# Optimization experiments

Hardware: AMD Instinct MI355X
Metric: run time of the kernel (lower is better)

Reference implementation:

```python
import jax, jax.numpy as jnp
import numpy as np

N, E, DIM = 50000, 1600000, 64
EPS = 1e-5


def setup_inputs() -> dict:
    key = jax.random.key(0)
    ks = jax.random.split(key, 12)
    s = 1.0 / np.sqrt(3 * DIM)
    s1 = 1.0 / np.sqrt(DIM)
    return {
        "x": jax.random.normal(ks[0], (N, DIM), dtype=jnp.float32),
        "edge_index": jax.random.randint(ks[1], (2, E), 0, N, dtype=jnp.int64),
        "edge_attr": jax.random.normal(ks[2], (E, DIM), dtype=jnp.float32),
        # gate_linear: Linear(3*dim, dim)
        "Wg": jax.random.uniform(ks[3], (3 * DIM, DIM), jnp.float32, -s, s),
        "bg": jax.random.uniform(ks[4], (DIM,), jnp.float32, -s, s),
        # src_linear / dst_linear: Linear(dim, dim)
        "Ws": jax.random.uniform(ks[5], (DIM, DIM), jnp.float32, -s1, s1),
        "bs": jax.random.uniform(ks[6], (DIM,), jnp.float32, -s1, s1),
        "Wd": jax.random.uniform(ks[7], (DIM, DIM), jnp.float32, -s1, s1),
        "bd": jax.random.uniform(ks[8], (DIM,), jnp.float32, -s1, s1),
        # BatchNorm affine params (track_running_stats=False -> batch stats)
        "gamma_n": 1.0 + 0.1 * jax.random.normal(ks[9], (DIM,), dtype=jnp.float32),
        "beta_n": 0.1 * jax.random.normal(ks[10], (DIM,), dtype=jnp.float32),
        "gamma_e": 1.0 + 0.1 * jax.random.normal(ks[11], (DIM,), dtype=jnp.float32),
        "beta_e": 0.1 * jax.random.normal(jax.random.fold_in(key, 99), (DIM,), dtype=jnp.float32),
    }


def batch_norm(h, gamma, beta):
    # BatchNorm1d with track_running_stats=False: batch mean, biased variance
    mu = jnp.mean(h, axis=0)
    var = jnp.mean((h - mu) ** 2, axis=0)
    return (h - mu) * jax.lax.rsqrt(var + EPS) * gamma + beta


def reference(x, edge_index, edge_attr, Wg, bg, Ws, bs, Wd, bd,
              gamma_n, beta_n, gamma_e, beta_e):
    src_idx, dst_idx = edge_index[0], edge_index[1]
    # gate: Linear(cat([x[src], x[dst], edge_attr])) -- split matmul == concat matmul
    d = x.shape[1]
    m = (x[src_idx] @ Wg[:d] + x[dst_idx] @ Wg[d:2 * d] + edge_attr @ Wg[2 * d:] + bg)  # [E, d]
    sigma = jax.nn.sigmoid(m / jnp.sqrt(jnp.float32(d)))
    src = x @ Ws + bs                              # [N, d]
    dst = (x @ Wd + bd)[dst_idx]                   # linear-then-gather == gather-then-linear
    agg = jax.ops.segment_sum(sigma * dst, src_idx, num_segments=x.shape[0])  # [N, d]
    h = src + agg
    node_out = jax.nn.relu(batch_norm(h, gamma_n, beta_n))
    edge_out = jax.nn.relu(batch_norm(m, gamma_e, beta_e))
    return (node_out, edge_out)
```

## Files before the change

### kernel.cpp

```cpp
#include <hip/hip_runtime.h>



__global__ __launch_bounds__(256, 2) void node_kernel(
    const float* __restrict__ x,
    const float* __restrict__ Wg,
    const float* __restrict__ Ws, const float* __restrict__ bs,
    const float* __restrict__ Wd, const float* __restrict__ bd,
    float* __restrict__ g0, float* __restrict__ g1,
    float* __restrict__ srcL, float* __restrict__ dstL,
    int N, int ntiles)
{
    __shared__ float ldsA[4][4096];
    const int lane = threadIdx.x & 63;
    const int wid  = threadIdx.x >> 6;
    float* lds = ldsA[wid];
    const int nw = gridDim.x * 4;
    const float bsv = bs[lane], bdv = bd[lane];

    for (int tile = blockIdx.x * 4 + wid; tile < ntiles; tile += nw) {
        const int r0 = tile * 64;
        {
            const int rb = lane >> 5, c2 = lane & 31;
            #pragma unroll
            for (int i = 0; i < 32; ++i) {
                int r = 2 * i + rb;
                int row = r0 + r; if (row >= N) row = N - 1;
                float2 v = *reinterpret_cast<const float2*>(x + (size_t)row * 64 + 2 * c2);
                int p = ((c2 + r) & 31) << 1;
                *reinterpret_cast<float2*>(&lds[r * 64 + p]) = v;
            }
        }
        float xr[64];
        #pragma unroll
        for (int kk = 0; kk < 32; ++kk) {
            int p = ((kk + lane) & 31) << 1;
            float2 v = *reinterpret_cast<const float2*>(&lds[lane * 64 + p]);
            xr[2 * kk] = v.x; xr[2 * kk + 1] = v.y;
        }
        #pragma unroll 1
        for (int mt = 0; mt < 4; ++mt) {
            const float* __restrict__ Wm = (mt == 0) ? Wg : (mt == 1) ? (Wg + 4096)
                                         : (mt == 2) ? Ws : Wd;
            #pragma unroll 1
            for (int ct = 0; ct < 2; ++ct) {
                float acc[32];
                #pragma unroll
                for (int c = 0; c < 32; ++c) acc[c] = 0.f;
                const float* __restrict__ Wp = Wm + ct * 32;
                #pragma unroll
                for (int k = 0; k < 64; ++k) {
                    float a = xr[k];
                    #pragma unroll
                    for (int c = 0; c < 32; ++c)
                        acc[c] = fmaf(a, Wp[k * 64 + c], acc[c]);
                }
                #pragma unroll
                for (int cc = 0; cc < 16; ++cc) {
                    int q = ct * 16 + cc;
                    int p = ((q + lane) & 31) << 1;
                    *reinterpret_cast<float2*>(&lds[lane * 64 + p]) =
                        make_float2(acc[2 * cc], acc[2 * cc + 1]);
                }
            }
            float bv = (mt == 2) ? bsv : (mt == 3) ? bdv : 0.f;
            float* __restrict__ op = (mt == 0) ? g0 : (mt == 1) ? g1 : (mt == 2) ? srcL : dstL;
            for (int j = 0; j < 64; ++j) {
                int row = r0 + j;
                if (row >= N) break;
                int p = ((((lane >> 1) + j) & 31) << 1) | (lane & 1);
                op[(size_t)row * 64 + lane] = lds[j * 64 + p] + bv;
            }
        }
    }
}

__global__ __launch_bounds__(256, 4) void edge_kernel(
    const float* __restrict__ ea, const int* __restrict__ eidx,
    const float* __restrict__ W2, const float* __restrict__ bg,
    const float* __restrict__ g0, const float* __restrict__ g1,
    const float* __restrict__ dstL, float* __restrict__ m_out,
    float* __restrict__ agg, float* __restrict__ stats,
    int E, int ntiles)
{
    __shared__ float lds[4096];
    const int tid  = threadIdx.x;
    const int lane = tid & 63;
    const int wid  = __builtin_amdgcn_readfirstlane(tid >> 6);
    const float bgv = bg[lane];
    float ssum = 0.f, ssq = 0.f;

    for (int tile = blockIdx.x; tile < ntiles; tile += gridDim.x) {
        const long e0 = (long)tile * 64;
        #pragma unroll
        for (int j = 0; j < 8; ++j) {
            int fp = tid + j * 256;
            int row = fp >> 5, c2 = fp & 31;
            long erow = e0 + row; if (erow >= E) erow = E - 1;
            float2 v = *reinterpret_cast<const float2*>(ea + erow * 64 + 2 * c2);
            int p = ((c2 + row) & 31) << 1;
            *reinterpret_cast<float2*>(&lds[row * 64 + p]) = v;
        }
        __syncthreads();
        float ear[64];
        #pragma unroll
        for (int kk = 0; kk < 32; ++kk) {
            int p = ((kk + lane) & 31) << 1;
            float2 v = *reinterpret_cast<const float2*>(&lds[lane * 64 + p]);
            ear[2 * kk] = v.x; ear[2 * kk + 1] = v.y;
        }
        __syncthreads();
        {
            float acc[16];
            #pragma unroll
            for (int c = 0; c < 16; ++c) acc[c] = 0.f;
            const float* __restrict__ Wp = W2 + wid * 16;
            #pragma unroll
            for (int k = 0; k < 64; ++k) {
                float a = ear[k];
                #pragma unroll
                for (int c = 0; c < 16; ++c)
                    acc[c] = fmaf(a, Wp[k * 64 + c], acc[c]);
            }
            #pragma unroll
            for (int cc = 0; cc < 8; ++cc) {
                int q = wid * 8 + cc;
                int p = ((q + lane) & 31) << 1;
                *reinterpret_cast<float2*>(&lds[lane * 64 + p]) =
                    make_float2(acc[2 * cc], acc[2 * cc + 1]);
            }
        }
        __syncthreads();
        #pragma unroll 4
        for (int i = 0; i < 16; ++i) {
            int j = wid * 16 + i;
            long e = e0 + j;
            if (e >= E) break;
            int s = eidx[e];
            int d = eidx[(long)E + e];
            int p = ((((lane >> 1) + j) & 31) << 1) | (lane & 1);
            float mv = lds[j * 64 + p];
            mv += bgv + g0[(size_t)s * 64 + lane] + g1[(size_t)d * 64 + lane];
            m_out[e * 64 + lane] = mv;
            ssum += mv;
            ssq = fmaf(mv, mv, ssq);
            float sg = __fdividef(1.f, 1.f + __expf(mv * -0.125f));
            atomicAdd(&agg[(size_t)s * 64 + lane], sg * dstL[(size_t)d * 64 + lane]);
        }
        __syncthreads();
    }
    atomicAdd(&stats[lane], ssum);
    atomicAdd(&stats[64 + lane], ssq);
}

__global__ void node_stats_kernel(const float* __restrict__ srcL, const float* __restrict__ agg,
                                  float* __restrict__ stats, int N)
{
    const int lane = threadIdx.x & 63;
    const int wid  = threadIdx.x >> 6;
    const int w = blockIdx.x * 4 + wid, nw = gridDim.x * 4;
    float s = 0.f, q = 0.f;
    for (int row = w; row < N; row += nw) {
        float h = srcL[(size_t)row * 64 + lane] + agg[(size_t)row * 64 + lane];
        s += h; q = fmaf(h, h, q);
    }
    atomicAdd(&stats[128 + lane], s);
    atomicAdd(&stats[192 + lane], q);
}

__global__ void finalize_kernel(float* __restrict__ stats,
                                const float* __restrict__ gn, const float* __restrict__ bn,
                                const float* __restrict__ ge, const float* __restrict__ be,
                                float invE, float invN)
{
    int c = threadIdx.x;
    float mu = stats[c] * invE;
    float var = stats[64 + c] * invE - mu * mu;
    float rs = rsqrtf(var + 1e-5f);
    float sc = rs * ge[c];
    stats[256 + c] = sc;
    stats[320 + c] = be[c] - mu * sc;
    mu = stats[128 + c] * invN;
    var = stats[192 + c] * invN - mu * mu;
    rs = rsqrtf(var + 1e-5f);
    sc = rs * gn[c];
    stats[384 + c] = sc;
    stats[448 + c] = bn[c] - mu * sc;
}

__global__ void edge_norm_kernel(float* __restrict__ mbuf, const float* __restrict__ stats, long n4)
{
    long i = (long)blockIdx.x * blockDim.x + threadIdx.x;
    const long stride = (long)gridDim.x * blockDim.x;
    int c4 = (int)(i & 15) * 4;
    float4 sc = *reinterpret_cast<const float4*>(&stats[256 + c4]);
    float4 sh = *reinterpret_cast<const float4*>(&stats[320 + c4]);
    float4* p = reinterpret_cast<float4*>(mbuf);
    for (; i < n4; i += stride) {
        float4 v = p[i];
        v.x = fmaxf(fmaf(v.x, sc.x, sh.x), 0.f);
        v.y = fmaxf(fmaf(v.y, sc.y, sh.y), 0.f);
        v.z = fmaxf(fmaf(v.z, sc.z, sh.z), 0.f);
        v.w = fmaxf(fmaf(v.w, sc.w, sh.w), 0.f);
        p[i] = v;
    }
}

__global__ void node_norm_kernel(const float* __restrict__ srcL, const float* __restrict__ agg,
                                 const float* __restrict__ stats, float* __restrict__ out, long n4)
{
    long i = (long)blockIdx.x * blockDim.x + threadIdx.x;
    const long stride = (long)gridDim.x * blockDim.x;
    int c4 = (int)(i & 15) * 4;
    float4 sc = *reinterpret_cast<const float4*>(&stats[384 + c4]);
    float4 sh = *reinterpret_cast<const float4*>(&stats[448 + c4]);
    const float4* a = reinterpret_cast<const float4*>(srcL);
    const float4* b = reinterpret_cast<const float4*>(agg);
    float4* o = reinterpret_cast<float4*>(out);
    for (; i < n4; i += stride) {
        float4 va = a[i], vb = b[i];
        float4 v;
        v.x = fmaxf(fmaf(va.x + vb.x, sc.x, sh.x), 0.f);
        v.y = fmaxf(fmaf(va.y + vb.y, sc.y, sh.y), 0.f);
        v.z = fmaxf(fmaf(va.z + vb.z, sc.z, sh.z), 0.f);
        v.w = fmaxf(fmaf(va.w + vb.w, sc.w, sh.w), 0.f);
        o[i] = v;
    }
}

extern "C" void kernel_launch(void* const* d_in, const int* in_sizes, int n_in,
                              void* d_out, int out_size, void* d_ws, size_t ws_size,
                              hipStream_t stream)
{
    const float* x    = (const float*)d_in[0];
    const int*   eidx = (const int*)d_in[1];
    const float* ea   = (const float*)d_in[2];
    const float* Wg   = (const float*)d_in[3];
    const float* bg   = (const float*)d_in[4];
    const float* Ws   = (const float*)d_in[5];
    const float* bs   = (const float*)d_in[6];
    const float* Wd   = (const float*)d_in[7];
    const float* bd   = (const float*)d_in[8];
    const float* gn   = (const float*)d_in[9];
    const float* bn   = (const float*)d_in[10];
    const float* ge   = (const float*)d_in[11];
    const float* be   = (const float*)d_in[12];

    const int N = in_sizes[0] / 64;
    const int E = in_sizes[2] / 64;

    float* ws    = (float*)d_ws;
    size_t nb    = (size_t)N * 64;
    float* g0    = ws;
    float* g1    = ws + nb;
    float* srcL  = ws + 2 * nb;
    float* dstL  = ws + 3 * nb;
    float* agg   = ws + 4 * nb;
    float* stats = ws + 5 * nb;

    float* node_out = (float*)d_out;
    float* m_out    = node_out + nb;

    hipMemsetAsync(agg, 0, nb * sizeof(float), stream);
    hipMemsetAsync(stats, 0, 512 * sizeof(float), stream);

    const int ntilesN = (N + 63) / 64;
    node_kernel<<<196, 256, 0, stream>>>(x, Wg, Ws, bs, Wd, bd, g0, g1, srcL, dstL, N, ntilesN);

    const int ntilesE = (E + 63) / 64;
    edge_kernel<<<2048, 256, 0, stream>>>(ea, eidx, Wg + 128 * 64, bg, g0, g1, dstL,
                                          m_out, agg, stats, E, ntilesE);

    node_stats_kernel<<<256, 256, 0, stream>>>(srcL, agg, stats, N);
    finalize_kernel<<<1, 64, 0, stream>>>(stats, gn, bn, ge, be, 1.f / (float)E, 1.f / (float)N);

    edge_norm_kernel<<<4096, 256, 0, stream>>>(m_out, stats, (long)E * 16);
    node_norm_kernel<<<1024, 256, 0, stream>>>(srcL, agg, stats, node_out, (long)N * 16);
}
```

Before: 1.279 ms.

## Vectorize edge kernel to float4 lanes with packed atomics and nontemporal streams

Reworks the edge kernel so each lane handles four channels of four edges at once, using 128-bit loads of g0/g1/dstL and packed two-wide float atomic adds into agg. It also drops the register staging of the edge_attr tile, adds nontemporal loads and stores for the streamed edge data and normalization pass, and reduces stats with shuffles before atomics. The tail check is removed and E/64 tiles are assumed, with a grid of 2500, so the code relies on E being divisible by 64. The node_stats kernel gains a stray zero-valued packed atomic with questionable operator precedence.

```diff
diff --git a/kernel.cpp b/kernel.cpp
--- a/kernel.cpp
+++ b/kernel.cpp
@@ -1,6 +1,18 @@
 #include <hip/hip_runtime.h>
 
 
+typedef float f4 __attribute__((ext_vector_type(4)));
+typedef float f2 __attribute__((ext_vector_type(2)));
+
+__device__ __forceinline__ void atomic_add2(float* p, float a, float b) {
+#if __has_builtin(__builtin_amdgcn_flat_atomic_fadd_v2f32)
+    f2 v = {a, b};
+    (void)__builtin_amdgcn_flat_atomic_fadd_v2f32(reinterpret_cast<f2*>(p), v);
+#else
+    (void)unsafeAtomicAdd(p, a);
+    (void)unsafeAtomicAdd(p + 1, b);
+#endif
+}
 
 __global__ __launch_bounds__(256, 2) void node_kernel(
     const float* __restrict__ x,
@@ -87,70 +99,90 @@
     const int tid  = threadIdx.x;
     const int lane = tid & 63;
     const int wid  = __builtin_amdgcn_readfirstlane(tid >> 6);
-    const float bgv = bg[lane];
-    float ssum = 0.f, ssq = 0.f;
+    const int q    = lane & 15;
+    const int rg   = lane >> 4;
+    const f4 bgv = *reinterpret_cast<const f4*>(bg + q * 4);
+    f4 ssum = {0.f, 0.f, 0.f, 0.f};
+    f4 ssq  = {0.f, 0.f, 0.f, 0.f};
 
     for (int tile = blockIdx.x; tile < ntiles; tile += gridDim.x) {
         const long e0 = (long)tile * 64;
         #pragma unroll
-        for (int j = 0; j < 8; ++j) {
+        for (int j = 0; j < 4; ++j) {
             int fp = tid + j * 256;
-            int row = fp >> 5, c2 = fp & 31;
-            long erow = e0 + row; if (erow >= E) erow = E - 1;
-            float2 v = *reinterpret_cast<const float2*>(ea + erow * 64 + 2 * c2);
-            int p = ((c2 + row) & 31) << 1;
-            *reinterpret_cast<float2*>(&lds[row * 64 + p]) = v;
+            int row = fp >> 4, qc = fp & 15;
+            f4 v = __builtin_nontemporal_load(
+                reinterpret_cast<const f4*>(ea + (e0 + row) * 64 + qc * 4));
+            int a4 = row * 16 + ((qc + row) & 15);
+            *reinterpret_cast<f4*>(&lds[a4 * 4]) = v;
         }
         __syncthreads();
-        float ear[64];
-        #pragma unroll
-        for (int kk = 0; kk < 32; ++kk) {
-            int p = ((kk + lane) & 31) << 1;
-            float2 v = *reinterpret_cast<const float2*>(&lds[lane * 64 + p]);
-            ear[2 * kk] = v.x; ear[2 * kk + 1] = v.y;
-        }
-        __syncthreads();
+        float acc[16];
+        #pragma unroll
+        for (int c = 0; c < 16; ++c) acc[c] = 0.f;
         {
-            float acc[16];
-            #pragma unroll
-            for (int c = 0; c < 16; ++c) acc[c] = 0.f;
             const float* __restrict__ Wp = W2 + wid * 16;
             #pragma unroll
-            for (int k = 0; k < 64; ++k) {
-                float a = ear[k];
+            for (int kk = 0; kk < 16; ++kk) {
+                int a4 = lane * 16 + ((kk + lane) & 15);
+                f4 a = *reinterpret_cast<const f4*>(&lds[a4 * 4]);
+                int k = kk * 4;
                 #pragma unroll
-                for (int c = 0; c < 16; ++c)
-                    acc[c] = fmaf(a, Wp[k * 64 + c], acc[c]);
+                for (int c = 0; c < 16; ++c) {
+                    acc[c] = fmaf(a.x, Wp[(k + 0) * 64 + c], acc[c]);
+                    acc[c] = fmaf(a.y, Wp[(k + 1) * 64 + c], acc[c]);
+                    acc[c] = fmaf(a.z, Wp[(k + 2) * 64 + c], acc[c]);
+                    acc[c] = fmaf(a.w, Wp[(k + 3) * 64 + c], acc[c]);
+                }
             }
-            #pragma unroll
-            for (int cc = 0; cc < 8; ++cc) {
-                int q = wid * 8 + cc;
-                int p = ((q + lane) & 31) << 1;
-                *reinterpret_cast<float2*>(&lds[lane * 64 + p]) =
-                    make_float2(acc[2 * cc], acc[2 * cc + 1]);
-            }
         }
         __syncthreads();
-        #pragma unroll 4
-        for (int i = 0; i < 16; ++i) {
-            int j = wid * 16 + i;
-            long e = e0 + j;
-            if (e >= E) break;
+        #pragma unroll
+        for (int cc = 0; cc < 4; ++cc) {
+            int qw = wid * 4 + cc;
+            int a4 = lane * 16 + ((qw + lane) & 15);
+            f4 w = {acc[4 * cc], acc[4 * cc + 1], acc[4 * cc + 2], acc[4 * cc + 3]};
+            *reinterpret_cast<f4*>(&lds[a4 * 4]) = w;
+        }
+        __syncthreads();
+        #pragma unroll
+        for (int i = 0; i < 4; ++i) {
+            int r = wid * 16 + i * 4 + rg;
+            long e = e0 + r;
             int s = eidx[e];
             int d = eidx[(long)E + e];
-            int p = ((((lane >> 1) + j) & 31) << 1) | (lane & 1);
-            float mv = lds[j * 64 + p];
-            mv += bgv + g0[(size_t)s * 64 + lane] + g1[(size_t)d * 64 + lane];
-            m_out[e * 64 + lane] = mv;
+            f4 mv = *reinterpret_cast<const f4*>(&lds[(r * 16 + ((q + r) & 15)) * 4]);
+            const f4 gs = *reinterpret_cast<const f4*>(g0 + (size_t)s * 64 + q * 4);
+            const f4 gd = *reinterpret_cast<const f4*>(g1 + (size_t)d * 64 + q * 4);
+            mv += bgv + gs + gd;
+            __builtin_nontemporal_store(mv, reinterpret_cast<f4*>(m_out + e * 64 + q * 4));
             ssum += mv;
-            ssq = fmaf(mv, mv, ssq);
-            float sg = __fdividef(1.f, 1.f + __expf(mv * -0.125f));
-            atomicAdd(&agg[(size_t)s * 64 + lane], sg * dstL[(size_t)d * 64 + lane]);
+            ssq.x = fmaf(mv.x, mv.x, ssq.x); ssq.y = fmaf(mv.y, mv.y, ssq.y);
+            ssq.z = fmaf(mv.z, mv.z, ssq.z); ssq.w = fmaf(mv.w, mv.w, ssq.w);
+            const f4 dl = *reinterpret_cast<const f4*>(dstL + (size_t)d * 64 + q * 4);
+            float c0 = __fdividef(dl.x, 1.f + __expf(mv.x * -0.125f));
+            float c1 = __fdividef(dl.y, 1.f + __expf(mv.y * -0.125f));
+            float c2 = __fdividef(dl.z, 1.f + __expf(mv.z * -0.125f));
+            float c3 = __fdividef(dl.w, 1.f + __expf(mv.w * -0.125f));
+            float* ap = agg + (size_t)s * 64 + q * 4;
+            atomic_add2(ap,     c0, c1);
+            atomic_add2(ap + 2, c2, c3);
         }
         __syncthreads();
     }
-    atomicAdd(&stats[lane], ssum);
-    atomicAdd(&stats[64 + lane], ssq);
+    #pragma unroll
+    for (int m = 16; m <= 32; m <<= 1) {
+        ssum.x += __shfl_xor(ssum.x, m); ssum.y += __shfl_xor(ssum.y, m);
+        ssum.z += __shfl_xor(ssum.z, m); ssum.w += __shfl_xor(ssum.w, m);
+        ssq.x  += __shfl_xor(ssq.x,  m); ssq.y  += __shfl_xor(ssq.y,  m);
+        ssq.z  += __shfl_xor(ssq.z,  m); ssq.w  += __shfl_xor(ssq.w,  m);
+    }
+    if (rg == 0) {
+        atomic_add2(stats + q * 4,          ssum.x, ssum.y);
+        atomic_add2(stats + q * 4 + 2,      ssum.z, ssum.w);
+        atomic_add2(stats + 64 + q * 4,     ssq.x,  ssq.y);
+        atomic_add2(stats + 64 + q * 4 + 2, ssq.z,  ssq.w);
+    }
 }
 
 __global__ void node_stats_kernel(const float* __restrict__ srcL, const float* __restrict__ agg,
@@ -164,8 +196,9 @@
         float h = srcL[(size_t)row * 64 + lane] + agg[(size_t)row * 64 + lane];
         s += h; q = fmaf(h, h, q);
     }
-    atomicAdd(&stats[128 + lane], s);
-    atomicAdd(&stats[192 + lane], q);
+    atomic_add2(&stats[128 + lane & ~1], 0.f, 0.f);
+    (void)unsafeAtomicAdd(&stats[128 + lane], s);
+    (void)unsafeAtomicAdd(&stats[192 + lane], q);
 }
 
 __global__ void finalize_kernel(float* __restrict__ stats,
@@ -193,16 +226,16 @@
     long i = (long)blockIdx.x * blockDim.x + threadIdx.x;
     const long stride = (long)gridDim.x * blockDim.x;
     int c4 = (int)(i & 15) * 4;
-    float4 sc = *reinterpret_cast<const float4*>(&stats[256 + c4]);
-    float4 sh = *reinterpret_cast<const float4*>(&stats[320 + c4]);
-    float4* p = reinterpret_cast<float4*>(mbuf);
+    f4 sc = *reinterpret_cast<const f4*>(&stats[256 + c4]);
+    f4 sh = *reinterpret_cast<const f4*>(&stats[320 + c4]);
+    f4* p = reinterpret_cast<f4*>(mbuf);
     for (; i < n4; i += stride) {
-        float4 v = p[i];
+        f4 v = __builtin_nontemporal_load(p + i);
         v.x = fmaxf(fmaf(v.x, sc.x, sh.x), 0.f);
         v.y = fmaxf(fmaf(v.y, sc.y, sh.y), 0.f);
         v.z = fmaxf(fmaf(v.z, sc.z, sh.z), 0.f);
         v.w = fmaxf(fmaf(v.w, sc.w, sh.w), 0.f);
-        p[i] = v;
+        __builtin_nontemporal_store(v, p + i);
     }
 }
 
@@ -212,18 +245,18 @@
     long i = (long)blockIdx.x * blockDim.x + threadIdx.x;
     const long stride = (long)gridDim.x * blockDim.x;
     int c4 = (int)(i & 15) * 4;
-    float4 sc = *reinterpret_cast<const float4*>(&stats[384 + c4]);
-    float4 sh = *reinterpret_cast<const float4*>(&stats[448 + c4]);
-    const float4* a = reinterpret_cast<const float4*>(srcL);
-    const float4* b = reinterpret_cast<const float4*>(agg);
-    float4* o = reinterpret_cast<float4*>(out);
+    f4 sc = *reinterpret_cast<const f4*>(&stats[384 + c4]);
+    f4 sh = *reinterpret_cast<const f4*>(&stats[448 + c4]);
+    const f4* a = reinterpret_cast<const f4*>(srcL);
+    const f4* b = reinterpret_cast<const f4*>(agg);
+    f4* o = reinterpret_cast<f4*>(out);
     for (; i < n4; i += stride) {
-        float4 va = a[i], vb = b[i];
-        float4 v;
-        v.x = fmaxf(fmaf(va.x + vb.x, sc.x, sh.x), 0.f);
-        v.y = fmaxf(fmaf(va.y + vb.y, sc.y, sh.y), 0.f);
-        v.z = fmaxf(fmaf(va.z + vb.z, sc.z, sh.z), 0.f);
-        v.w = fmaxf(fmaf(va.w + vb.w, sc.w, sh.w), 0.f);
+        f4 va = a[i], vb = b[i];
+        f4 v = va + vb;
+        v.x = fmaxf(fmaf(v.x, sc.x, sh.x), 0.f);
+        v.y = fmaxf(fmaf(v.y, sc.y, sh.y), 0.f);
+        v.z = fmaxf(fmaf(v.z, sc.z, sh.z), 0.f);
+        v.w = fmaxf(fmaf(v.w, sc.w, sh.w), 0.f);
         o[i] = v;
     }
 }
@@ -261,14 +294,14 @@
     float* node_out = (float*)d_out;
     float* m_out    = node_out + nb;
 
-    hipMemsetAsync(agg, 0, nb * sizeof(float), stream);
-    hipMemsetAsync(stats, 0, 512 * sizeof(float), stream);
+    (void)hipMemsetAsync(agg, 0, nb * sizeof(float), stream);
+    (void)hipMemsetAsync(stats, 0, 512 * sizeof(float), stream);
 
     const int ntilesN = (N + 63) / 64;
     node_kernel<<<196, 256, 0, stream>>>(x, Wg, Ws, bs, Wd, bd, g0, g1, srcL, dstL, N, ntilesN);
 
-    const int ntilesE = (E + 63) / 64;
-    edge_kernel<<<2048, 256, 0, stream>>>(ea, eidx, Wg + 128 * 64, bg, g0, g1, dstL,
+    const int ntilesE = E / 64;
+    edge_kernel<<<2500, 256, 0, stream>>>(ea, eidx, Wg + 128 * 64, bg, g0, g1, dstL,
                                           m_out, agg, stats, E, ntilesE);
 
     node_stats_kernel<<<256, 256, 0, stream>>>(srcL, agg, stats, N);
```

Result: slower. 2.991 ms (+133.9%).
